# Kernel optimization log

Hardware: AMD Instinct MI355X
Metric: run time of the kernel (lower is better)

## Reference

```python
import jax, jax.numpy as jnp
import numpy as np

WS = 7; SHIFT = 3; HEADS = 4; DIM = 192; C2 = 2 * DIM; HD = C2 // HEADS
H = W = 60
PAD = (WS - H % WS) % WS          # 3
HP = H + PAD; WP = W + PAD        # 63
NW = (HP // WS) * (WP // WS)      # 81 windows
N = WS * WS                       # 49 tokens per window
MLP_H = int(4.0 * C2)             # 1536


def _rel_pos_index():
    coords = np.stack(np.meshgrid(np.arange(WS), np.arange(WS), indexing='ij'))
    cf = coords.reshape(2, -1)
    rel = (cf[:, :, None] - cf[:, None, :]).transpose(1, 2, 0)
    rel[:, :, 0] += WS - 1
    rel[:, :, 1] += WS - 1
    rel[:, :, 0] *= 2 * WS - 1
    return rel.sum(-1)  # (N, N) into table of size (2*WS-1)^2


def _attn_mask():
    img = np.zeros((HP, WP))
    cnt = 0
    for hs in (slice(0, -WS), slice(-WS, -SHIFT), slice(-SHIFT, None)):
        for ws_ in (slice(0, -WS), slice(-WS, -SHIFT), slice(-SHIFT, None)):
            img[hs, ws_] = cnt; cnt += 1
    mw = img.reshape(HP // WS, WS, WP // WS, WS).transpose(0, 2, 1, 3).reshape(-1, N)
    diff = mw[:, None, :] - mw[:, :, None]
    return np.where(diff != 0, -100.0, 0.0).astype(np.float32)  # (NW, N, N)

REL_IDX = jnp.asarray(_rel_pos_index().reshape(-1))
ATTN_MASK = jnp.asarray(_attn_mask())


def layernorm(x, w, b, eps=1e-5):
    mu = jnp.mean(x, axis=-1, keepdims=True)
    var = jnp.var(x, axis=-1, keepdims=True)
    return (x - mu) * jax.lax.rsqrt(var + eps) * w + b


def setup_inputs() -> dict:
    key = jax.random.key(0)
    ks = jax.random.split(key, 16)
    s = 0.02
    return {
        'x': jax.random.normal(ks[0], (8, DIM, H, W), jnp.float32),
        'g': jax.random.normal(ks[1], (8, DIM, H, W), jnp.float32),
        'norm_w': jnp.ones((C2,), jnp.float32),
        'norm_b': jnp.zeros((C2,), jnp.float32),
        'n1_w': jnp.ones((C2,), jnp.float32),
        'n1_b': jnp.zeros((C2,), jnp.float32),
        'qkv_w': jax.random.normal(ks[2], (3 * C2, C2), jnp.float32) * s,
        'qkv_b': jnp.zeros((3 * C2,), jnp.float32),
        'proj_w': jax.random.normal(ks[3], (C2, C2), jnp.float32) * s,
        'proj_b': jnp.zeros((C2,), jnp.float32),
        'rpb': jax.random.normal(ks[4], ((2 * WS - 1) ** 2, HEADS), jnp.float32) * s,
        'n2_w': jnp.ones((C2,), jnp.float32),
        'n2_b': jnp.zeros((C2,), jnp.float32),
        'fc1_w': jax.random.normal(ks[5], (MLP_H, C2), jnp.float32) * s,
        'fc1_b': jnp.zeros((MLP_H,), jnp.float32),
        'fc2_w': jax.random.normal(ks[6], (C2, MLP_H), jnp.float32) * s,
        'fc2_b': jnp.zeros((C2,), jnp.float32),
        'conv_w': jax.random.normal(ks[7], (DIM, C2, 3, 3), jnp.float32) * s,
        'conv_b': jnp.zeros((DIM,), jnp.float32),
    }


def reference(x, g, norm_w, norm_b, n1_w, n1_b, qkv_w, qkv_b, proj_w, proj_b,
              rpb, n2_w, n2_b, fc1_w, fc1_b, fc2_w, fc2_b, conv_w, conv_b):
    B = x.shape[0]
    # concat + NCHW -> NHWC + pad to window multiple
    comb = jnp.concatenate([x, g], axis=1).transpose(0, 2, 3, 1)   # (B,H,W,2C)
    comb = jnp.pad(comb, ((0, 0), (0, PAD), (0, PAD), (0, 0)))     # (B,HP,WP,2C)
    z = layernorm(comb, norm_w, norm_b)
    # ---- Swin block ----
    shortcut = z
    zn = layernorm(z, n1_w, n1_b)
    zn = jnp.roll(zn, shift=(-SHIFT, -SHIFT), axis=(1, 2))
    # window partition -> (B*NW, N, 2C)
    w = zn.reshape(B, HP // WS, WS, WP // WS, WS, C2).transpose(0, 1, 3, 2, 4, 5)
    w = w.reshape(B * NW, N, C2)
    qkv = (w @ qkv_w.T + qkv_b).reshape(B * NW, N, 3, HEADS, HD).transpose(2, 0, 3, 1, 4)
    q, k, v = qkv[0], qkv[1], qkv[2]                               # (B*NW,H,N,HD)
    attn = jnp.einsum('bhnd,bhmd->bhnm', q, k) * (HD ** -0.5)
    bias = rpb[REL_IDX].reshape(N, N, HEADS).transpose(2, 0, 1)    # (H,N,N)
    attn = attn + bias[None]
    attn = attn.reshape(B, NW, HEADS, N, N) + ATTN_MASK[None, :, None]
    attn = jax.nn.softmax(attn.reshape(B * NW, HEADS, N, N), axis=-1)
    out = jnp.einsum('bhnm,bhmd->bhnd', attn, v).transpose(0, 2, 1, 3).reshape(B * NW, N, C2)
    out = out @ proj_w.T + proj_b
    # window reverse + unshift
    out = out.reshape(B, HP // WS, WP // WS, WS, WS, C2).transpose(0, 1, 3, 2, 4, 5)
    out = out.reshape(B, HP, WP, C2)
    out = jnp.roll(out, shift=(SHIFT, SHIFT), axis=(1, 2))
    z = shortcut + out
    h = layernorm(z, n2_w, n2_b)
    h = jax.nn.gelu(h @ fc1_w.T + fc1_b, approximate=False)
    z = z + (h @ fc2_w.T + fc2_b)
    # crop, NHWC -> NCHW, 3x3 reduce conv, residual
    z = z[:, :H, :W, :].transpose(0, 3, 1, 2)                      # (B,2C,H,W)
    red = jax.lax.conv_general_dilated(
        z, conv_w, window_strides=(1, 1), padding=((1, 1), (1, 1)),
        dimension_numbers=('NCHW', 'OIHW', 'NCHW')) + conv_b[None, :, None, None]
    return red + x
```

## Files before the change

kernel.cpp:

```cpp
#include <hip/hip_runtime.h>
#include <cstddef>
#include <cstdint>

#define HEADS   4
#define C2c     384
#define HPc     63
#define WPc     63
#define NWc     81
#define BATCH   8
#define TOKP    (BATCH*HPc*WPc)
#define TOKC    (BATCH*60*60)
#define MLPH    1536
#define TPB     3969
#define CONVK   3456
#define CONVN   192

typedef __attribute__((ext_vector_type(8))) short short8;
typedef __attribute__((ext_vector_type(4))) float f32x4;
typedef unsigned short u16;

__device__ __forceinline__ u16 f2bf(float f) {
  unsigned u = __float_as_uint(f);
  u += 0x7fff + ((u >> 16) & 1);
  return (u16)(u >> 16);
}
__device__ __forceinline__ float bf2f(u16 b) { return __uint_as_float((unsigned)b << 16); }

#define GLOAD16(gp, lp) __builtin_amdgcn_global_load_lds( \
    (const __attribute__((address_space(1))) unsigned*)(gp), \
    (__attribute__((address_space(3))) unsigned*)(lp), 16, 0, 0)

__device__ __forceinline__ int xcd_swizzle(int orig, int nwg) {
  int q = nwg >> 3, r = nwg & 7;
  int xcd = orig & 7, off = orig >> 3;
  return (xcd < r ? xcd*(q+1) : r*(q+1) + (xcd - r)*q) + off;
}

__device__ __forceinline__ float2 block_reduce_384(float v, float* red) {
  __syncthreads();
  float s = v, q = v * v;
  #pragma unroll
  for (int o = 32; o > 0; o >>= 1) {
    s += __shfl_down(s, o);
    q += __shfl_down(q, o);
  }
  int w = threadIdx.x >> 6;
  if ((threadIdx.x & 63) == 0) { red[2*w] = s; red[2*w+1] = q; }
  __syncthreads();
  float ts = red[0]+red[2]+red[4]+red[6]+red[8]+red[10];
  float tq = red[1]+red[3]+red[5]+red[7]+red[9]+red[11];
  return make_float2(ts, tq);
}

__global__ __launch_bounds__(384)
void k1a_kernel(const float* __restrict__ x, const float* __restrict__ g,
                const float* __restrict__ nw, const float* __restrict__ nb,
                const float* __restrict__ n1w, const float* __restrict__ n1b,
                float* __restrict__ musig, u16* __restrict__ wbuf)
{
  __shared__ float red[12];
  int t = blockIdx.x;
  int b = t / (HPc*WPc);
  int rem = t - b*(HPc*WPc);
  int i = rem / WPc, j = rem - (rem / WPc)*WPc;
  int c = threadIdx.x;

  float v = 0.f;
  if (i < 60 && j < 60) {
    if (c < 192) v = x[(((size_t)b*192 + c)*60 + i)*60 + j];
    else         v = g[(((size_t)b*192 + (c-192))*60 + i)*60 + j];
  }
  float2 ss = block_reduce_384(v, red);
  float mu  = ss.x * (1.f/384.f);
  float var = ss.y * (1.f/384.f) - mu*mu;
  float rs  = rsqrtf(var + 1e-5f);
  if (c == 0) { musig[2*t] = mu; musig[2*t+1] = rs; }
  float zi  = (v - mu) * rs * nw[c] + nb[c];
  float2 s2 = block_reduce_384(zi, red);
  float mu2  = s2.x * (1.f/384.f);
  float var2 = s2.y * (1.f/384.f) - mu2*mu2;
  float zn = (zi - mu2) * rsqrtf(var2 + 1e-5f) * n1w[c] + n1b[c];
  int ai = i - 3; if (ai < 0) ai += HPc;
  int aj = j - 3; if (aj < 0) aj += WPc;
  int win = (ai/7)*9 + (aj/7);
  int tok = (ai%7)*7 + (aj%7);
  wbuf[(((size_t)b*NWc + win)*49 + tok)*C2c + c] = f2bf(zn);
}

__global__ __launch_bounds__(384)
void k1b_kernel(const float* __restrict__ x, const float* __restrict__ g,
                const float* __restrict__ nw, const float* __restrict__ nb,
                const float* __restrict__ musig, float* __restrict__ z)
{
  int tc = blockIdx.x;
  int b = tc / 3600;
  int rem = tc - b*3600;
  int i = rem / 60, j = rem - (rem/60)*60;
  int t = b*(HPc*WPc) + i*WPc + j;
  int c = threadIdx.x;
  float v;
  if (c < 192) v = x[(((size_t)b*192 + c)*60 + i)*60 + j];
  else         v = g[(((size_t)b*192 + (c-192))*60 + i)*60 + j];
  float mu = musig[2*t], rs = musig[2*t+1];
  z[(size_t)tc*C2c + c] = (v - mu) * rs * nw[c] + nb[c];
}

__global__ __launch_bounds__(384)
void ln2_kernel(const float* __restrict__ z, const float* __restrict__ nw,
                const float* __restrict__ nb, u16* __restrict__ out)
{
  __shared__ float red[12];
  int tc = blockIdx.x;
  int c = threadIdx.x;
  float v = z[(size_t)tc*C2c + c];
  float2 ss = block_reduce_384(v, red);
  float mu  = ss.x * (1.f/384.f);
  float var = ss.y * (1.f/384.f) - mu*mu;
  out[(size_t)tc*C2c + c] = f2bf((v - mu) * rsqrtf(var + 1e-5f) * nw[c] + nb[c]);
}

__global__ __launch_bounds__(256)
void f2bf_kernel(const float* __restrict__ in, u16* __restrict__ out, int n4)
{
  int t = blockIdx.x*256 + threadIdx.x;
  if (t >= n4) return;
  float4 v = ((const float4*)in)[t];
  ushort4 o;
  o.x = f2bf(v.x); o.y = f2bf(v.y); o.z = f2bf(v.z); o.w = f2bf(v.w);
  ((ushort4*)out)[t] = o;
}

__global__ void zero_kernel(uint4* p) { p[threadIdx.x] = make_uint4(0,0,0,0); }

__global__ void split_convw(const float* __restrict__ cw, u16* __restrict__ hi, u16* __restrict__ lo)
{
  int t = blockIdx.x*blockDim.x + threadIdx.x;
  if (t >= CONVN*CONVK) return;
  int oc = t / CONVK, k = t - oc*CONVK;
  int p = k / 384, c = k - p*384;
  float v = cw[((size_t)oc*384 + c)*9 + p];
  u16 h = f2bf(v);
  hi[t] = h;
  lo[t] = f2bf(v - bf2f(h));
}

template<int EPI>
__global__ __launch_bounds__(256)
void mfma_gemm(const u16* __restrict__ A, const u16* __restrict__ B,
               const float* __restrict__ bias, u16* __restrict__ Cb, float* __restrict__ zbuf,
               int M, int N, int K, int ldb, int addbias)
{
  __shared__ u16 As [128*64];
  __shared__ u16 Bs [128*64];
  int tid = threadIdx.x;
  int lane = tid & 63, w = tid >> 6;
  int wr = w >> 1, wc = w & 1;
  int nwg = gridDim.x * gridDim.y;
  int swz = xcd_swizzle(blockIdx.y*gridDim.x + blockIdx.x, nwg);
  int bx = swz % gridDim.x, by = swz / gridDim.x;
  int m0 = by * 128, n0 = bx * 128;
  int srow = lane >> 3, sslot = (lane & 7) ^ srow;

  f32x4 acc[4][4];
  #pragma unroll
  for (int i = 0; i < 4; ++i)
    #pragma unroll
    for (int j = 0; j < 4; ++j) acc[i][j] = (f32x4){0.f,0.f,0.f,0.f};

  char* AsB = (char*)As; char* BsB = (char*)Bs;
  int r15 = lane & 15, kq = lane >> 4;

  for (int k0 = 0; k0 < K; k0 += 64) {
    #pragma unroll
    for (int i = 0; i < 4; ++i) {
      int rblk = w*4 + i;
      int ar = m0 + rblk*8 + srow; if (ar >= M) ar = M - 1;
      int br = n0 + rblk*8 + srow;
      GLOAD16(A + (size_t)ar*K   + k0 + sslot*8, AsB + rblk*1024);
      GLOAD16(B + (size_t)br*ldb + k0 + sslot*8, BsB + rblk*1024);
    }
    __syncthreads();
    #pragma unroll
    for (int ks = 0; ks < 2; ++ks) {
      int slog = ks*4 + kq;
      short8 af[4], bf[4];
      #pragma unroll
      for (int mi = 0; mi < 4; ++mi) {
        int row = wr*64 + mi*16 + r15;
        af[mi] = *(const short8*)(AsB + row*128 + ((slog ^ (row&7))<<4));
      }
      #pragma unroll
      for (int ni = 0; ni < 4; ++ni) {
        int row = wc*64 + ni*16 + r15;
        bf[ni] = *(const short8*)(BsB + row*128 + ((slog ^ (row&7))<<4));
      }
      #pragma unroll
      for (int mi = 0; mi < 4; ++mi)
        #pragma unroll
        for (int ni = 0; ni < 4; ++ni)
          acc[mi][ni] = __builtin_amdgcn_mfma_f32_16x16x32_bf16(af[mi], bf[ni], acc[mi][ni], 0, 0, 0);
    }
    __syncthreads();
  }

  int fq = lane >> 4, fr = lane & 15;
  #pragma unroll
  for (int mi = 0; mi < 4; ++mi) {
    #pragma unroll
    for (int j = 0; j < 4; ++j) {
      int m = m0 + wr*64 + mi*16 + fq*4 + j;
      if (m >= M) continue;
      int zrow = 0; bool zok = true;
      if (EPI == 1) {
        int b = m / TPB;
        int rem = m - b*TPB;
        int win = rem / 49, tok = rem - (rem/49)*49;
        int wh = win/9, ww = win - (win/9)*9;
        int th = tok/7, tw = tok - (tok/7)*7;
        int oi = wh*7 + th + 3; if (oi >= HPc) oi -= HPc;
        int oj = ww*7 + tw + 3; if (oj >= WPc) oj -= WPc;
        zok = (oi < 60 && oj < 60);
        zrow = (b*60 + oi)*60 + oj;
      }
      #pragma unroll
      for (int ni = 0; ni < 4; ++ni) {
        int n = n0 + wc*64 + ni*16 + fr;
        float val = acc[mi][ni][j];
        if (EPI == 0) {
          Cb[(size_t)m*N + n] = f2bf(val + bias[n]);
        } else if (EPI == 1) {
          if (zok) zbuf[(size_t)zrow*C2c + n] += val + bias[n];
        } else if (EPI == 2) {
          float vv = val + bias[n];
          float ge = 0.5f*vv*(1.f + erff(vv*0.70710678118654752f));
          Cb[(size_t)m*N + n] = f2bf(ge);
        } else if (EPI == 3) {
          float vv = val + (addbias ? bias[n] : 0.f);
          zbuf[(size_t)m*C2c + n] += vv;
        } else {
          float vv = val + (addbias ? bias[n] : 0.f) + zbuf[(size_t)m*C2c + n];
          zbuf[(size_t)m*C2c + n] = vv;
          Cb[(size_t)m*C2c + n] = f2bf(vv);
        }
      }
    }
  }
}

__global__ __launch_bounds__(256)
void mfma_conv(const u16* __restrict__ Y, const u16* __restrict__ Bh, const u16* __restrict__ Bl,
               const float* __restrict__ cb, const float* __restrict__ xres,
               const u16* __restrict__ zpad, float* __restrict__ outp)
{
  __shared__ u16 As [64*128];
  __shared__ u16 Bsh[64*128];
  __shared__ u16 Bsl[64*128];
  int tid = threadIdx.x;
  int lane = tid & 63, w = tid >> 6;
  int wr = w >> 1, wc = w & 1;
  int nwg = gridDim.x * gridDim.y;
  int swz = xcd_swizzle(blockIdx.y*gridDim.x + blockIdx.x, nwg);
  int bx = swz % 3, by = swz / 3;
  int m0 = by * 64, n0 = bx * 64;
  int l4 = lane >> 4;

  f32x4 acc[2][2];
  #pragma unroll
  for (int i = 0; i < 2; ++i)
    #pragma unroll
    for (int j = 0; j < 2; ++j) acc[i][j] = (f32x4){0.f,0.f,0.f,0.f};

  int pbA[4], ohA[4], owA[4], ssA[4], cA[4];
  #pragma unroll
  for (int i = 0; i < 4; ++i) {
    cA[i] = i*4 + w;
    int row = cA[i]*4 + l4;
    int pix = m0 + row;
    int pb = pix / 3600;
    int prem = pix - pb*3600;
    pbA[i] = pb; ohA[i] = prem / 60; owA[i] = prem - (prem/60)*60;
    ssA[i] = (lane & 15) ^ (row & 7);
  }
  int brB[4], ssB[4], cB[4];
  #pragma unroll
  for (int j = 0; j < 4; ++j) {
    cB[j] = j*4 + w;
    int row = cB[j]*4 + l4;
    brB[j] = n0 + row;
    ssB[j] = (lane & 15) ^ (row & 7);
  }

  char* AsB = (char*)As; char* BhB = (char*)Bsh; char* BlB = (char*)Bsl;
  int r15 = lane & 15, kq = lane >> 4;

  for (int k0 = 0; k0 < CONVK; k0 += 128) {
    int p  = k0 / 384;
    int c0 = k0 - p*384;
    int dh = p/3 - 1, dw = (p - (p/3)*3) - 1;
    #pragma unroll
    for (int j = 0; j < 4; ++j) {
      GLOAD16(Bh + (size_t)brB[j]*CONVK + k0 + ssB[j]*8, BhB + cB[j]*1024);
      GLOAD16(Bl + (size_t)brB[j]*CONVK + k0 + ssB[j]*8, BlB + cB[j]*1024);
    }
    #pragma unroll
    for (int i = 0; i < 4; ++i) {
      int ih = ohA[i] + dh, iw = owA[i] + dw;
      const u16* src = ((unsigned)ih < 60u && (unsigned)iw < 60u)
        ? Y + ((size_t)pbA[i]*3600 + ih*60 + iw)*C2c + c0 + ssA[i]*8
        : zpad;
      GLOAD16(src, AsB + cA[i]*1024);
    }
    __syncthreads();
    #pragma unroll
    for (int ks = 0; ks < 4; ++ks) {
      int slog = ks*4 + kq;
      short8 af[2], bh[2], bl[2];
      #pragma unroll
      for (int mi = 0; mi < 2; ++mi) {
        int row = wr*32 + mi*16 + r15;
        af[mi] = *(const short8*)(AsB + row*256 + ((slog ^ (row&7))<<4));
      }
      #pragma unroll
      for (int ni = 0; ni < 2; ++ni) {
        int row = wc*32 + ni*16 + r15;
        int off = row*256 + ((slog ^ (row&7))<<4);
        bh[ni] = *(const short8*)(BhB + off);
        bl[ni] = *(const short8*)(BlB + off);
      }
      #pragma unroll
      for (int mi = 0; mi < 2; ++mi)
        #pragma unroll
        for (int ni = 0; ni < 2; ++ni) {
          acc[mi][ni] = __builtin_amdgcn_mfma_f32_16x16x32_bf16(af[mi], bh[ni], acc[mi][ni], 0, 0, 0);
          acc[mi][ni] = __builtin_amdgcn_mfma_f32_16x16x32_bf16(af[mi], bl[ni], acc[mi][ni], 0, 0, 0);
        }
    }
    __syncthreads();
  }

  int fq = lane >> 4, fr = lane & 15;
  #pragma unroll
  for (int mi = 0; mi < 2; ++mi) {
    #pragma unroll
    for (int j = 0; j < 4; ++j) {
      int m = m0 + wr*32 + mi*16 + fq*4 + j;
      int pb = m / 3600;
      int rem = m - pb*3600;
      int oh = rem / 60, ow = rem - (rem/60)*60;
      #pragma unroll
      for (int ni = 0; ni < 2; ++ni) {
        int oc = n0 + wc*32 + ni*16 + fr;
        size_t oi = ((size_t)pb*192 + oc)*3600 + oh*60 + ow;
        outp[oi] = acc[mi][ni][j] + cb[oc] + xres[oi];
      }
    }
  }
}

#define QS_STRIDE 100
#define VS_STRIDE 104
#define SS_STRIDE 53

__global__ __launch_bounds__(256)
void attn_kernel(const u16* __restrict__ qkv, const float* __restrict__ rpb,
                 u16* __restrict__ out)
{
  __shared__ float qs[52*QS_STRIDE];
  __shared__ float ks[52*QS_STRIDE];
  __shared__ float S[52*SS_STRIDE];
  int blk = blockIdx.x;
  int h   = blk & 3;
  int bw  = blk >> 2;
  int win = bw % NWc;
  const u16* base = qkv + (size_t)bw*49*1152;
  int tid = threadIdx.x;

  for (int t2 = tid; t2 < 588; t2 += 256) {
    int r = t2 / 12, dq = t2 - (t2/12)*12;
    short8 qv = *(const short8*)(base + r*1152 +       h*96 + dq*8);
    short8 kv = *(const short8*)(base + r*1152 + 384 + h*96 + dq*8);
    #pragma unroll
    for (int e = 0; e < 8; ++e) {
      qs[r*QS_STRIDE + dq*8 + e] = bf2f((u16)qv[e]);
      ks[r*QS_STRIDE + dq*8 + e] = bf2f((u16)kv[e]);
    }
  }
  __syncthreads();

  const float scale = 0.1020620726159657f;
  int wh = win / 9, ww = win - (win/9)*9;

  if (tid < 169) {
    int tr = tid / 13, tc = tid - (tid/13)*13;
    int r0 = tr*4, c0 = tc*4;
    float a[4][4] = {};
    for (int k0 = 0; k0 < 96; k0 += 4) {
      float4 qv[4], kv4[4];
      #pragma unroll
      for (int i = 0; i < 4; ++i) qv[i]  = *(const float4*)&qs[(r0+i)*QS_STRIDE + k0];
      #pragma unroll
      for (int j = 0; j < 4; ++j) kv4[j] = *(const float4*)&ks[(c0+j)*QS_STRIDE + k0];
      #pragma unroll
      for (int i = 0; i < 4; ++i)
        #pragma unroll
        for (int j = 0; j < 4; ++j)
          a[i][j] += qv[i].x*kv4[j].x + qv[i].y*kv4[j].y + qv[i].z*kv4[j].z + qv[i].w*kv4[j].w;
    }
    #pragma unroll
    for (int i = 0; i < 4; ++i) {
      int r = r0 + i;
      if (r < 49) {
        int r1 = r/7, c1 = r - (r/7)*7;
        int hp1 = wh*7 + r1, wp1 = ww*7 + c1;
        int g1 = (hp1 < 56 ? 0 : (hp1 < 60 ? 1 : 2))*3 + (wp1 < 56 ? 0 : (wp1 < 60 ? 1 : 2));
        #pragma unroll
        for (int j = 0; j < 4; ++j) {
          int c = c0 + j;
          if (c < 49) {
            int r2 = c/7, c2 = c - (c/7)*7;
            float s = a[i][j]*scale + rpb[((r1 - r2 + 6)*13 + (c1 - c2 + 6))*HEADS + h];
            int hp2 = wh*7 + r2, wp2 = ww*7 + c2;
            int g2 = (hp2 < 56 ? 0 : (hp2 < 60 ? 1 : 2))*3 + (wp2 < 56 ? 0 : (wp2 < 60 ? 1 : 2));
            if (g1 != g2) s -= 100.f;
            S[r*SS_STRIDE + c] = s;
          }
        }
      }
    }
  }
  __syncthreads();

  for (int t2 = tid; t2 < 588; t2 += 256) {
    int r = t2 / 12, dq = t2 - (t2/12)*12;
    short8 vv = *(const short8*)(base + r*1152 + 768 + h*96 + dq*8);
    #pragma unroll
    for (int e = 0; e < 8; ++e) ks[r*VS_STRIDE + dq*8 + e] = bf2f((u16)vv[e]);
  }
  if (tid < 49) {
    float mx = -1e30f;
    for (int c = 0; c < 49; ++c) mx = fmaxf(mx, S[tid*SS_STRIDE + c]);
    float sum = 0.f;
    for (int c = 0; c < 49; ++c) { float e = expf(S[tid*SS_STRIDE + c] - mx); S[tid*SS_STRIDE + c] = e; sum += e; }
    float inv = 1.f / sum;
    for (int c = 0; c < 49; ++c) S[tid*SS_STRIDE + c] *= inv;
  }
  __syncthreads();

  if (tid < 156) {
    int tr2 = tid / 12, tc2 = tid - (tid/12)*12;
    int r0 = tr2*4, d0 = tc2*8;
    float o[4][8] = {};
    for (int c = 0; c < 49; ++c) {
      float4 v0 = *(const float4*)&ks[c*VS_STRIDE + d0];
      float4 v1 = *(const float4*)&ks[c*VS_STRIDE + d0 + 4];
      #pragma unroll
      for (int i = 0; i < 4; ++i) {
        float sv = S[(r0+i)*SS_STRIDE + c];
        o[i][0] += sv*v0.x; o[i][1] += sv*v0.y; o[i][2] += sv*v0.z; o[i][3] += sv*v0.w;
        o[i][4] += sv*v1.x; o[i][5] += sv*v1.y; o[i][6] += sv*v1.z; o[i][7] += sv*v1.w;
      }
    }
    #pragma unroll
    for (int i = 0; i < 4; ++i) {
      int r = r0 + i;
      if (r >= 49) continue;
      ushort4 w0, w1;
      w0.x = f2bf(o[i][0]); w0.y = f2bf(o[i][1]); w0.z = f2bf(o[i][2]); w0.w = f2bf(o[i][3]);
      w1.x = f2bf(o[i][4]); w1.y = f2bf(o[i][5]); w1.z = f2bf(o[i][6]); w1.w = f2bf(o[i][7]);
      size_t ob = ((size_t)bw*49 + r)*C2c + h*96 + d0;
      *(ushort4*)&out[ob]     = w0;
      *(ushort4*)&out[ob + 4] = w1;
    }
  }
}

extern "C" void kernel_launch(void* const* d_in, const int* in_sizes, int n_in,
                              void* d_out, int out_size, void* d_ws, size_t ws_size,
                              hipStream_t stream)
{
  const float* x      = (const float*)d_in[0];
  const float* g      = (const float*)d_in[1];
  const float* norm_w = (const float*)d_in[2];
  const float* norm_b = (const float*)d_in[3];
  const float* n1_w   = (const float*)d_in[4];
  const float* n1_b   = (const float*)d_in[5];
  const float* qkv_w  = (const float*)d_in[6];
  const float* qkv_b  = (const float*)d_in[7];
  const float* proj_w = (const float*)d_in[8];
  const float* proj_b = (const float*)d_in[9];
  const float* rpb    = (const float*)d_in[10];
  const float* n2_w   = (const float*)d_in[11];
  const float* n2_b   = (const float*)d_in[12];
  const float* fc1_w  = (const float*)d_in[13];
  const float* fc1_b  = (const float*)d_in[14];
  const float* fc2_w  = (const float*)d_in[15];
  const float* fc2_b  = (const float*)d_in[16];
  const float* conv_w = (const float*)d_in[17];
  const float* conv_b = (const float*)d_in[18];
  float* outp = (float*)d_out;

  char* p = (char*)d_ws;
  u16* wbuf = (u16*)p;              p += (size_t)TOKP*C2c*2;
  char* qr  = p;                    p += (size_t)TOKP*1152*2;
  u16*   qkvb = (u16*)qr;
  float* z    = (float*)qr;
  u16*   hid_c = (u16*)(qr + (size_t)TOKC*C2c*4);
  u16* qkvw = (u16*)p; p += 442368*2;
  u16* pw   = (u16*)p; p += 147456*2;
  u16* f1w  = (u16*)p; p += 589824*2;
  u16* f2w  = (u16*)p; p += 589824*2;
  u16* cvwh = (u16*)p; p += (size_t)CONVN*CONVK*2;
  u16* cvwl = (u16*)p; p += (size_t)CONVN*CONVK*2;
  float* musig = (float*)p; p += (size_t)TOKP*2*4;
  u16* zpad = (u16*)p; p += 256;
  u16* hid_f = (u16*)p;
  size_t need_full = (size_t)(p - (char*)d_ws) + (size_t)TOKC*MLPH*2;
  bool full_mlp = ws_size >= need_full;

  f2bf_kernel<<<(442368/4 + 255)/256, 256, 0, stream>>>(qkv_w, qkvw, 442368/4);
  f2bf_kernel<<<(147456/4 + 255)/256, 256, 0, stream>>>(proj_w, pw, 147456/4);
  f2bf_kernel<<<(589824/4 + 255)/256, 256, 0, stream>>>(fc1_w, f1w, 589824/4);
  f2bf_kernel<<<(589824/4 + 255)/256, 256, 0, stream>>>(fc2_w, f2w, 589824/4);
  split_convw<<<(CONVN*CONVK + 255)/256, 256, 0, stream>>>(conv_w, cvwh, cvwl);
  zero_kernel<<<1, 16, 0, stream>>>((uint4*)zpad);

  k1a_kernel<<<TOKP, 384, 0, stream>>>(x, g, norm_w, norm_b, n1_w, n1_b, musig, wbuf);

  mfma_gemm<0><<<dim3(9, 249), 256, 0, stream>>>(
      wbuf, qkvw, qkv_b, qkvb, nullptr, TOKP, 1152, 384, 384, 1);

  attn_kernel<<<BATCH*NWc*HEADS, 256, 0, stream>>>(qkvb, rpb, wbuf);

  k1b_kernel<<<TOKC, 384, 0, stream>>>(x, g, norm_w, norm_b, musig, z);

  mfma_gemm<1><<<dim3(3, 249), 256, 0, stream>>>(
      wbuf, pw, proj_b, nullptr, z, TOKP, 384, 384, 384, 1);

  ln2_kernel<<<TOKC, 384, 0, stream>>>(z, n2_w, n2_b, wbuf);

  if (full_mlp) {
    mfma_gemm<2><<<dim3(12, 225), 256, 0, stream>>>(
        wbuf, f1w, fc1_b, hid_f, nullptr, TOKC, MLPH, 384, 384, 1);
    mfma_gemm<4><<<dim3(3, 225), 256, 0, stream>>>(
        hid_f, f2w, fc2_b, wbuf, z, TOKC, 384, MLPH, MLPH, 1);
  } else {
    const int CH = 9600;
    for (int off = 0; off < TOKC; off += CH) {
      mfma_gemm<2><<<dim3(12, 75), 256, 0, stream>>>(
          wbuf + (size_t)off*C2c, f1w, fc1_b, hid_c, nullptr, CH, MLPH, 384, 384, 1);
      mfma_gemm<4><<<dim3(3, 75), 256, 0, stream>>>(
          hid_c, f2w, fc2_b, wbuf + (size_t)off*C2c, z + (size_t)off*C2c, CH, 384, MLPH, MLPH, 1);
    }
  }

  mfma_conv<<<dim3(3, 450), 256, 0, stream>>>(wbuf, cvwh, cvwl, conv_b, x, zpad, outp);
}
```

Baseline: 745.4 us.

## Merge weight-prep kernels, split MLP along hidden dim, retile conv LDS into K halves

Replaces the four bf16-conversion launches, the conv weight split and the zeroing kernel with a single prep kernel. The MLP now runs as four hidden-dimension slices of 384, each an fc1 GEMM into a smaller hidden buffer followed by an fc2 GEMM that accumulates into z, with the last slice also writing bf16. This removes the large full hidden buffer and the chunked fallback. The conv kernel's shared-memory tiles are reorganised into two 64-wide K halves with a new swizzle, and the final fc2 epilogue no longer writes z back. The cost is more, smaller GEMM launches and extra fp32 read-modify-write traffic on z.

```diff
diff --git a/kernel.cpp b/kernel.cpp
--- a/kernel.cpp
+++ b/kernel.cpp
@@ -120,28 +120,33 @@
 }
 
 __global__ __launch_bounds__(256)
-void f2bf_kernel(const float* __restrict__ in, u16* __restrict__ out, int n4)
+void prep_kernel(const float* __restrict__ qkv_w, const float* __restrict__ proj_w,
+                 const float* __restrict__ fc1_w, const float* __restrict__ fc2_w,
+                 const float* __restrict__ conv_w,
+                 u16* __restrict__ qkvw, u16* __restrict__ pw,
+                 u16* __restrict__ f1w, u16* __restrict__ f2w,
+                 u16* __restrict__ cvwh, u16* __restrict__ cvwl, u16* __restrict__ zpad)
 {
   int t = blockIdx.x*256 + threadIdx.x;
-  if (t >= n4) return;
-  float4 v = ((const float4*)in)[t];
-  ushort4 o;
-  o.x = f2bf(v.x); o.y = f2bf(v.y); o.z = f2bf(v.z); o.w = f2bf(v.w);
-  ((ushort4*)out)[t] = o;
-}
-
-__global__ void zero_kernel(uint4* p) { p[threadIdx.x] = make_uint4(0,0,0,0); }
-
-__global__ void split_convw(const float* __restrict__ cw, u16* __restrict__ hi, u16* __restrict__ lo)
-{
-  int t = blockIdx.x*blockDim.x + threadIdx.x;
-  if (t >= CONVN*CONVK) return;
-  int oc = t / CONVK, k = t - oc*CONVK;
-  int p = k / 384, c = k - p*384;
-  float v = cw[((size_t)oc*384 + c)*9 + p];
-  u16 h = f2bf(v);
-  hi[t] = h;
-  lo[t] = f2bf(v - bf2f(h));
+  if (t < 442368) { qkvw[t] = f2bf(qkv_w[t]); return; }
+  t -= 442368;
+  if (t < 147456) { pw[t] = f2bf(proj_w[t]); return; }
+  t -= 147456;
+  if (t < 589824) { f1w[t] = f2bf(fc1_w[t]); return; }
+  t -= 589824;
+  if (t < 589824) { f2w[t] = f2bf(fc2_w[t]); return; }
+  t -= 589824;
+  if (t < CONVN*CONVK) {
+    int oc = t / CONVK, k = t - oc*CONVK;
+    int p = k / 384, c = k - p*384;
+    float v = conv_w[((size_t)oc*384 + c)*9 + p];
+    u16 h = f2bf(v);
+    cvwh[t] = h;
+    cvwl[t] = f2bf(v - bf2f(h));
+    return;
+  }
+  t -= CONVN*CONVK;
+  if (t < 128) zpad[t] = 0;
 }
 
 template<int EPI>
@@ -239,7 +244,6 @@
           zbuf[(size_t)m*C2c + n] += vv;
         } else {
           float vv = val + (addbias ? bias[n] : 0.f) + zbuf[(size_t)m*C2c + n];
-          zbuf[(size_t)m*C2c + n] = vv;
           Cb[(size_t)m*C2c + n] = f2bf(vv);
         }
       }
@@ -252,9 +256,9 @@
                const float* __restrict__ cb, const float* __restrict__ xres,
                const u16* __restrict__ zpad, float* __restrict__ outp)
 {
-  __shared__ u16 As [64*128];
-  __shared__ u16 Bsh[64*128];
-  __shared__ u16 Bsl[64*128];
+  __shared__ u16 As [2*64*64];
+  __shared__ u16 Bsh[2*64*64];
+  __shared__ u16 Bsl[2*64*64];
   int tid = threadIdx.x;
   int lane = tid & 63, w = tid >> 6;
   int wr = w >> 1, wc = w & 1;
@@ -262,7 +266,7 @@
   int swz = xcd_swizzle(blockIdx.y*gridDim.x + blockIdx.x, nwg);
   int bx = swz % 3, by = swz / 3;
   int m0 = by * 64, n0 = bx * 64;
-  int l4 = lane >> 4;
+  int srow = lane >> 3, sslot = (lane & 7) ^ srow;
 
   f32x4 acc[2][2];
   #pragma unroll
@@ -270,24 +274,23 @@
     #pragma unroll
     for (int j = 0; j < 2; ++j) acc[i][j] = (f32x4){0.f,0.f,0.f,0.f};
 
-  int pbA[4], ohA[4], owA[4], ssA[4], cA[4];
+  int pbA[4], ohA[4], owA[4], colA[4], cA[4];
   #pragma unroll
   for (int i = 0; i < 4; ++i) {
-    cA[i] = i*4 + w;
-    int row = cA[i]*4 + l4;
+    cA[i] = w + i*4;
+    int row = (cA[i] & 7)*8 + srow;
     int pix = m0 + row;
     int pb = pix / 3600;
     int prem = pix - pb*3600;
     pbA[i] = pb; ohA[i] = prem / 60; owA[i] = prem - (prem/60)*60;
-    ssA[i] = (lane & 15) ^ (row & 7);
-  }
-  int brB[4], ssB[4], cB[4];
+    colA[i] = (cA[i] >> 3)*64 + sslot*8;
+  }
+  int brB[4], colB[4], cB[4];
   #pragma unroll
   for (int j = 0; j < 4; ++j) {
-    cB[j] = j*4 + w;
-    int row = cB[j]*4 + l4;
-    brB[j] = n0 + row;
-    ssB[j] = (lane & 15) ^ (row & 7);
+    cB[j] = w + j*4;
+    brB[j] = n0 + (cB[j] & 7)*8 + srow;
+    colB[j] = (cB[j] >> 3)*64 + sslot*8;
   }
 
   char* AsB = (char*)As; char* BhB = (char*)Bsh; char* BlB = (char*)Bsl;
@@ -299,41 +302,44 @@
     int dh = p/3 - 1, dw = (p - (p/3)*3) - 1;
     #pragma unroll
     for (int j = 0; j < 4; ++j) {
-      GLOAD16(Bh + (size_t)brB[j]*CONVK + k0 + ssB[j]*8, BhB + cB[j]*1024);
-      GLOAD16(Bl + (size_t)brB[j]*CONVK + k0 + ssB[j]*8, BlB + cB[j]*1024);
+      GLOAD16(Bh + (size_t)brB[j]*CONVK + k0 + colB[j], BhB + cB[j]*1024);
+      GLOAD16(Bl + (size_t)brB[j]*CONVK + k0 + colB[j], BlB + cB[j]*1024);
     }
     #pragma unroll
     for (int i = 0; i < 4; ++i) {
       int ih = ohA[i] + dh, iw = owA[i] + dw;
       const u16* src = ((unsigned)ih < 60u && (unsigned)iw < 60u)
-        ? Y + ((size_t)pbA[i]*3600 + ih*60 + iw)*C2c + c0 + ssA[i]*8
+        ? Y + ((size_t)pbA[i]*3600 + ih*60 + iw)*C2c + c0 + colA[i]
         : zpad;
       GLOAD16(src, AsB + cA[i]*1024);
     }
     __syncthreads();
     #pragma unroll
-    for (int ks = 0; ks < 4; ++ks) {
-      int slog = ks*4 + kq;
-      short8 af[2], bh[2], bl[2];
-      #pragma unroll
-      for (int mi = 0; mi < 2; ++mi) {
-        int row = wr*32 + mi*16 + r15;
-        af[mi] = *(const short8*)(AsB + row*256 + ((slog ^ (row&7))<<4));
-      }
-      #pragma unroll
-      for (int ni = 0; ni < 2; ++ni) {
-        int row = wc*32 + ni*16 + r15;
-        int off = row*256 + ((slog ^ (row&7))<<4);
-        bh[ni] = *(const short8*)(BhB + off);
-        bl[ni] = *(const short8*)(BlB + off);
-      }
-      #pragma unroll
-      for (int mi = 0; mi < 2; ++mi)
+    for (int h = 0; h < 2; ++h) {
+      #pragma unroll
+      for (int ks = 0; ks < 2; ++ks) {
+        int slog = ks*4 + kq;
+        short8 af[2], bh2[2], bl2[2];
+        #pragma unroll
+        for (int mi = 0; mi < 2; ++mi) {
+          int row = wr*32 + mi*16 + r15;
+          af[mi] = *(const short8*)(AsB + h*8192 + row*128 + ((slog ^ (row&7))<<4));
+        }
         #pragma unroll
         for (int ni = 0; ni < 2; ++ni) {
-          acc[mi][ni] = __builtin_amdgcn_mfma_f32_16x16x32_bf16(af[mi], bh[ni], acc[mi][ni], 0, 0, 0);
-          acc[mi][ni] = __builtin_amdgcn_mfma_f32_16x16x32_bf16(af[mi], bl[ni], acc[mi][ni], 0, 0, 0);
+          int row = wc*32 + ni*16 + r15;
+          int off = h*8192 + row*128 + ((slog ^ (row&7))<<4);
+          bh2[ni] = *(const short8*)(BhB + off);
+          bl2[ni] = *(const short8*)(BlB + off);
         }
+        #pragma unroll
+        for (int mi = 0; mi < 2; ++mi)
+          #pragma unroll
+          for (int ni = 0; ni < 2; ++ni) {
+            acc[mi][ni] = __builtin_amdgcn_mfma_f32_16x16x32_bf16(af[mi], bh2[ni], acc[mi][ni], 0, 0, 0);
+            acc[mi][ni] = __builtin_amdgcn_mfma_f32_16x16x32_bf16(af[mi], bl2[ni], acc[mi][ni], 0, 0, 0);
+          }
+      }
     }
     __syncthreads();
   }
@@ -500,11 +506,6 @@
   float* outp = (float*)d_out;
 
   char* p = (char*)d_ws;
-  u16* wbuf = (u16*)p;              p += (size_t)TOKP*C2c*2;
-  char* qr  = p;                    p += (size_t)TOKP*1152*2;
-  u16*   qkvb = (u16*)qr;
-  float* z    = (float*)qr;
-  u16*   hid_c = (u16*)(qr + (size_t)TOKC*C2c*4);
   u16* qkvw = (u16*)p; p += 442368*2;
   u16* pw   = (u16*)p; p += 147456*2;
   u16* f1w  = (u16*)p; p += 589824*2;
@@ -513,16 +514,14 @@
   u16* cvwl = (u16*)p; p += (size_t)CONVN*CONVK*2;
   float* musig = (float*)p; p += (size_t)TOKP*2*4;
   u16* zpad = (u16*)p; p += 256;
-  u16* hid_f = (u16*)p;
-  size_t need_full = (size_t)(p - (char*)d_ws) + (size_t)TOKC*MLPH*2;
-  bool full_mlp = ws_size >= need_full;
-
-  f2bf_kernel<<<(442368/4 + 255)/256, 256, 0, stream>>>(qkv_w, qkvw, 442368/4);
-  f2bf_kernel<<<(147456/4 + 255)/256, 256, 0, stream>>>(proj_w, pw, 147456/4);
-  f2bf_kernel<<<(589824/4 + 255)/256, 256, 0, stream>>>(fc1_w, f1w, 589824/4);
-  f2bf_kernel<<<(589824/4 + 255)/256, 256, 0, stream>>>(fc2_w, f2w, 589824/4);
-  split_convw<<<(CONVN*CONVK + 255)/256, 256, 0, stream>>>(conv_w, cvwh, cvwl);
-  zero_kernel<<<1, 16, 0, stream>>>((uint4*)zpad);
+  u16* wbuf = (u16*)p; p += (size_t)TOKP*C2c*2;
+  char* qr  = p;       p += (size_t)TOKP*1152*2;
+  u16*   qkvb = (u16*)qr;
+  float* z    = (float*)qr;
+  u16*   hid  = (u16*)(qr + (size_t)TOKC*C2c*4);
+
+  prep_kernel<<<9505, 256, 0, stream>>>(qkv_w, proj_w, fc1_w, fc2_w, conv_w,
+                                        qkvw, pw, f1w, f2w, cvwh, cvwl, zpad);
 
   k1a_kernel<<<TOKP, 384, 0, stream>>>(x, g, norm_w, norm_b, n1_w, n1_b, musig, wbuf);
 
@@ -538,19 +537,15 @@
 
   ln2_kernel<<<TOKC, 384, 0, stream>>>(z, n2_w, n2_b, wbuf);
 
-  if (full_mlp) {
-    mfma_gemm<2><<<dim3(12, 225), 256, 0, stream>>>(
-        wbuf, f1w, fc1_b, hid_f, nullptr, TOKC, MLPH, 384, 384, 1);
-    mfma_gemm<4><<<dim3(3, 225), 256, 0, stream>>>(
-        hid_f, f2w, fc2_b, wbuf, z, TOKC, 384, MLPH, MLPH, 1);
-  } else {
-    const int CH = 9600;
-    for (int off = 0; off < TOKC; off += CH) {
-      mfma_gemm<2><<<dim3(12, 75), 256, 0, stream>>>(
-          wbuf + (size_t)off*C2c, f1w, fc1_b, hid_c, nullptr, CH, MLPH, 384, 384, 1);
-      mfma_gemm<4><<<dim3(3, 75), 256, 0, stream>>>(
-          hid_c, f2w, fc2_b, wbuf + (size_t)off*C2c, z + (size_t)off*C2c, CH, 384, MLPH, MLPH, 1);
-    }
+  for (int h0 = 0; h0 < MLPH; h0 += 384) {
+    mfma_gemm<2><<<dim3(3, 225), 256, 0, stream>>>(
+        wbuf, f1w + (size_t)h0*384, fc1_b + h0, hid, nullptr, TOKC, 384, 384, 384, 1);
+    if (h0 < MLPH - 384)
+      mfma_gemm<3><<<dim3(3, 225), 256, 0, stream>>>(
+          hid, f2w + h0, fc2_b, nullptr, z, TOKC, 384, 384, MLPH, h0 == 0 ? 1 : 0);
+    else
+      mfma_gemm<4><<<dim3(3, 225), 256, 0, stream>>>(
+          hid, f2w + h0, fc2_b, wbuf, z, TOKC, 384, 384, MLPH, 0);
   }
 
   mfma_conv<<<dim3(3, 450), 256, 0, stream>>>(wbuf, cvwh, cvwl, conv_b, x, zpad, outp);
```

After: 868.6 us. +16.5%, slower.
